# Kernel tuning notes

Measured on AMD Instinct MI355X. Metric: run time of the kernel, lower is better.

Reference implementation:

```python
import jax, jax.numpy as jnp
import numpy as np

B, S, D, H = 2, 2048, 1024, 16
DH = D // H  # 64


def setup_inputs() -> dict:
    key = jax.random.key(0)
    ks = jax.random.split(key, 9)
    def rn(k, shape, scale=1.0):
        return jax.random.normal(k, shape, dtype=jnp.float32) * scale
    w_scale = 1.0 / np.sqrt(D)
    return {
        "queries": rn(ks[0], (B, S, D)),
        "keys": rn(ks[1], (B, S, D)),
        "values": rn(ks[2], (B, S, D)),
        "Wq": rn(ks[3], (D, D), w_scale),
        "bq": rn(ks[4], (D,), w_scale),
        "Wk": rn(ks[5], (D, D), w_scale),
        "bk": rn(ks[6], (D,), w_scale),
        "Wv": rn(ks[7], (D, D), w_scale),
        "bv": rn(ks[8], (D,), w_scale),
    }


def _split_heads(x):
    # torch: cat(split(x, DH, dim=-1), dim=0) -> index (h*B + b); equivalent to
    # [B,S,H,DH] -> [H,B,S,DH]
    bsz, slen, _ = x.shape
    return x.reshape(bsz, slen, H, DH).transpose(2, 0, 1, 3)


def reference(queries, keys, values, Wq, bq, Wk, bk, Wv, bv):
    # Linear projections (W stored so that y = x @ W + b)
    Q = queries @ Wq + bq
    K = keys @ Wk + bk
    V = values @ Wv + bv

    Qh = _split_heads(Q)  # [H,B,S,DH]
    Kh = _split_heads(K)
    Vh = _split_heads(V)

    scale = 1.0 / jnp.sqrt(jnp.asarray(DH, dtype=Qh.dtype))
    scores = jnp.einsum("hbqd,hbkd->hbqk", Qh, Kh) * scale  # [H,B,S,S]
    attn = jax.nn.softmax(scores, axis=-1)  # dropout_rate=0 -> identity
    out = jnp.einsum("hbqk,hbkd->hbqd", attn, Vh)  # [H,B,S,DH]

    # torch: cat(split(out, B, dim=0), dim=2) -> [B,S,H*DH] with head h in slice h
    out = out.transpose(1, 2, 0, 3).reshape(queries.shape[0], queries.shape[1], D)
    return out + queries  # residual; NOTE: W_O is defined but unused in the original forward
```

## Files before the change

### kernel.cpp

```cpp
#include <hip/hip_runtime.h>
#include <hip/hip_bf16.h>
#include <math.h>

#define BB 2
#define SS 2048
#define DD 1024
#define HH 16
#define DHH 64
#define MM (BB * SS)

typedef float f32x4 __attribute__((ext_vector_type(4)));
typedef __bf16 bf16x8 __attribute__((ext_vector_type(8)));

#define N_QKV ((size_t)MM * DD)
#define N_W   ((size_t)DD * DD)

__device__ unsigned short g_X [3][N_QKV];
__device__ unsigned short g_Q [N_QKV];
__device__ unsigned short g_K [N_QKV];
__device__ unsigned short g_Vt[N_QKV];
__device__ unsigned short g_Wt[3][N_W];

__device__ __forceinline__ unsigned short f2bu(float f) {
    unsigned u = __float_as_uint(f);
    unsigned r = u + 0x7FFFu + ((u >> 16) & 1u);
    return (unsigned short)(r >> 16);
}

union FragU { uint4 u; bf16x8 v; unsigned short s[8]; };
static __device__ __forceinline__ bf16x8 ldfrag(const unsigned short* p) {
    FragU f; f.u = *(const uint4*)p; return f.v;
}

__global__ __launch_bounds__(256) void cvt3(
        const float* __restrict__ x0, const float* __restrict__ x1,
        const float* __restrict__ x2, unsigned short* __restrict__ X)
{
    const float* src = blockIdx.y == 0 ? x0 : (blockIdx.y == 1 ? x1 : x2);
    unsigned short* dst = X + (size_t)blockIdx.y * N_QKV;
    const size_t i = ((size_t)blockIdx.x * 256 + threadIdx.x) * 4;
    const float4 v = *(const float4*)(src + i);
    ushort4 s;
    s.x = f2bu(v.x); s.y = f2bu(v.y); s.z = f2bu(v.z); s.w = f2bu(v.w);
    *(ushort4*)(dst + i) = s;
}

__global__ __launch_bounds__(256) void transpose_w3(
        const float* __restrict__ W0, const float* __restrict__ W1,
        const float* __restrict__ W2, unsigned short* __restrict__ Wt3)
{
    const float* W = blockIdx.z == 0 ? W0 : (blockIdx.z == 1 ? W1 : W2);
    unsigned short* Wt = Wt3 + (size_t)blockIdx.z * N_W;
    __shared__ float Ts[64][65];
    const int t = threadIdx.x;
    const int k0 = blockIdx.y * 64, n0 = blockIdx.x * 64;
#pragma unroll
    for (int i = 0; i < 16; ++i) {
        const int f = t + 256 * i, r = f >> 6, c = f & 63;
        Ts[r][c] = W[(size_t)(k0 + r) * DD + n0 + c];
    }
    __syncthreads();
#pragma unroll
    for (int i = 0; i < 16; ++i) {
        const int f = t + 256 * i, r = f >> 6, c = f & 63;
        Wt[(size_t)(n0 + r) * DD + k0 + c] = f2bu(Ts[c][r]);
    }
}

__global__ __launch_bounds__(256) void proj3(
        const unsigned short* __restrict__ X, const unsigned short* __restrict__ Wt3,
        const float* __restrict__ bq, const float* __restrict__ bk,
        const float* __restrict__ bv,
        unsigned short* __restrict__ Qp, unsigned short* __restrict__ Kp,
        unsigned short* __restrict__ Vtp)
{
    const int z = blockIdx.z;
    const unsigned short* xb = X   + (size_t)z * N_QKV;
    const unsigned short* Wt = Wt3 + (size_t)z * N_W;
    const float* bias = z == 0 ? bq : (z == 1 ? bk : bv);
    const float scale = z == 0 ? 0.125f : 1.0f;

    __shared__ unsigned short As[128][72];
    __shared__ unsigned short Bs[128][72];
    const int t = threadIdx.x, lane = t & 63, w = t >> 6;
    const int q = lane >> 4, li = lane & 15;
    const int wm = (w >> 1) * 64, wn = (w & 1) * 64;
    const int m0 = blockIdx.y * 128, n0 = blockIdx.x * 128;
    const int rs = t >> 3, cs = (t & 7) * 8;

    f32x4 acc[4][4];
#pragma unroll
    for (int mt = 0; mt < 4; ++mt)
#pragma unroll
        for (int nt = 0; nt < 4; ++nt) acc[mt][nt] = (f32x4)0.f;

    uint4 pa0, pa1, pa2, pa3, pb0, pb1, pb2, pb3;
#define PROJ_LD(kk) \
    pa0 = *(const uint4*)(xb + (size_t)(m0 + rs      ) * DD + (kk) + cs); \
    pa1 = *(const uint4*)(xb + (size_t)(m0 + rs + 32 ) * DD + (kk) + cs); \
    pa2 = *(const uint4*)(xb + (size_t)(m0 + rs + 64 ) * DD + (kk) + cs); \
    pa3 = *(const uint4*)(xb + (size_t)(m0 + rs + 96 ) * DD + (kk) + cs); \
    pb0 = *(const uint4*)(Wt + (size_t)(n0 + rs      ) * DD + (kk) + cs); \
    pb1 = *(const uint4*)(Wt + (size_t)(n0 + rs + 32 ) * DD + (kk) + cs); \
    pb2 = *(const uint4*)(Wt + (size_t)(n0 + rs + 64 ) * DD + (kk) + cs); \
    pb3 = *(const uint4*)(Wt + (size_t)(n0 + rs + 96 ) * DD + (kk) + cs);

    PROJ_LD(0)

    for (int kk = 0; kk < DD; kk += 64) {
        *(uint4*)&As[rs     ][cs] = pa0;
        *(uint4*)&As[rs + 32][cs] = pa1;
        *(uint4*)&As[rs + 64][cs] = pa2;
        *(uint4*)&As[rs + 96][cs] = pa3;
        *(uint4*)&Bs[rs     ][cs] = pb0;
        *(uint4*)&Bs[rs + 32][cs] = pb1;
        *(uint4*)&Bs[rs + 64][cs] = pb2;
        *(uint4*)&Bs[rs + 96][cs] = pb3;
        __syncthreads();
        if (kk + 64 < DD) { PROJ_LD(kk + 64) }
#pragma unroll
        for (int ks = 0; ks < 64; ks += 32) {
            bf16x8 a[4], b[4];
#pragma unroll
            for (int mt = 0; mt < 4; ++mt) a[mt] = ldfrag(&As[wm + mt * 16 + li][ks + q * 8]);
#pragma unroll
            for (int nt = 0; nt < 4; ++nt) b[nt] = ldfrag(&Bs[wn + nt * 16 + li][ks + q * 8]);
#pragma unroll
            for (int mt = 0; mt < 4; ++mt)
#pragma unroll
                for (int nt = 0; nt < 4; ++nt)
                    acc[mt][nt] = __builtin_amdgcn_mfma_f32_16x16x32_bf16(
                        a[mt], b[nt], acc[mt][nt], 0, 0, 0);
        }
        __syncthreads();
    }
#undef PROJ_LD

    float bvv[4];
#pragma unroll
    for (int nt = 0; nt < 4; ++nt) bvv[nt] = bias[n0 + wn + nt * 16 + li];

    if (z < 2) {
        unsigned short* out = z == 0 ? Qp : Kp;
#pragma unroll
        for (int mt = 0; mt < 4; ++mt)
#pragma unroll
            for (int nt = 0; nt < 4; ++nt)
#pragma unroll
                for (int reg = 0; reg < 4; ++reg) {
                    const int m = m0 + wm + mt * 16 + q * 4 + reg;
                    out[(size_t)m * DD + n0 + wn + nt * 16 + li] =
                        f2bu((acc[mt][nt][reg] + bvv[nt]) * scale);
                }
    } else {
        const int b = m0 >> 11;
        const int h = (n0 + wn) >> 6;
#pragma unroll
        for (int mt = 0; mt < 4; ++mt)
#pragma unroll
            for (int nt = 0; nt < 4; ++nt) {
                const int s = (m0 & (SS - 1)) + wm + mt * 16 + q * 4;
                const int dh = nt * 16 + li;
                ushort4 sv;
                sv.x = f2bu(acc[mt][nt][0] + bvv[nt]);
                sv.y = f2bu(acc[mt][nt][1] + bvv[nt]);
                sv.z = f2bu(acc[mt][nt][2] + bvv[nt]);
                sv.w = f2bu(acc[mt][nt][3] + bvv[nt]);
                *(ushort4*)(Vtp + ((size_t)((b * HH + h) * DHH + dh)) * SS + s) = sv;
            }
    }
}

__global__ __launch_bounds__(256) void attn4(
        const unsigned short* __restrict__ Qg, const unsigned short* __restrict__ Kg,
        const unsigned short* __restrict__ Vtg,
        const float* __restrict__ queries, float* __restrict__ outp)
{
    __shared__ unsigned short QP [128][72];
    __shared__ unsigned short Ks [64][72];
    __shared__ unsigned short Vts[64][72];

    const int t = threadIdx.x, lane = t & 63, w = t >> 6;
    const int q = lane >> 4, li = lane & 15;
    const int qt = blockIdx.x, h = blockIdx.y, b = blockIdx.z;
    const int rs = t >> 3, cs = (t & 7) * 8;

    {
        const unsigned short* qsrc = Qg + (size_t)(b * SS + qt * 128) * DD + h * DHH + cs;
        *(uint4*)&QP[rs      ][cs] = *(const uint4*)(qsrc + (size_t)(rs      ) * DD);
        *(uint4*)&QP[rs + 32 ][cs] = *(const uint4*)(qsrc + (size_t)(rs + 32 ) * DD);
        *(uint4*)&QP[rs + 64 ][cs] = *(const uint4*)(qsrc + (size_t)(rs + 64 ) * DD);
        *(uint4*)&QP[rs + 96 ][cs] = *(const uint4*)(qsrc + (size_t)(rs + 96 ) * DD);
    }

    uint4 pk0, pk1, pv0, pv1;
#define ATTN_LD(s0) \
    pk0 = *(const uint4*)(Kg  + (size_t)(b * SS + (s0) + rs) * DD + h * DHH + cs); \
    pk1 = *(const uint4*)(Kg  + (size_t)(b * SS + (s0) + rs + 32) * DD + h * DHH + cs); \
    pv0 = *(const uint4*)(Vtg + ((size_t)((b * HH + h) * DHH + rs)) * SS + (s0) + cs); \
    pv1 = *(const uint4*)(Vtg + ((size_t)((b * HH + h) * DHH + rs + 32)) * SS + (s0) + cs);

    ATTN_LD(0)
    *(uint4*)&Ks [rs     ][cs] = pk0;
    *(uint4*)&Ks [rs + 32][cs] = pk1;
    *(uint4*)&Vts[rs     ][cs] = pv0;
    *(uint4*)&Vts[rs + 32][cs] = pv1;
    __syncthreads();

    bf16x8 qa[2][2];
#pragma unroll
    for (int mt = 0; mt < 2; ++mt)
#pragma unroll
        for (int ki = 0; ki < 2; ++ki)
            qa[mt][ki] = ldfrag(&QP[w * 32 + mt * 16 + li][ki * 32 + q * 8]);

    FragU ones;
#pragma unroll
    for (int j = 0; j < 8; ++j) ones.s[j] = 0x3F80;

    f32x4 o[2][4], lacc[2];
#pragma unroll
    for (int mt = 0; mt < 2; ++mt) {
        lacc[mt] = (f32x4)0.f;
#pragma unroll
        for (int nt = 0; nt < 4; ++nt) o[mt][nt] = (f32x4)0.f;
    }

    for (int kt = 0; kt < SS / 64; ++kt) {
        if (kt + 1 < SS / 64) { ATTN_LD((kt + 1) * 64) }

        f32x4 sc[2][4];
#pragma unroll
        for (int mt = 0; mt < 2; ++mt)
#pragma unroll
            for (int nt = 0; nt < 4; ++nt) sc[mt][nt] = (f32x4)0.f;
#pragma unroll
        for (int ki = 0; ki < 2; ++ki) {
            bf16x8 bb[4];
#pragma unroll
            for (int nt = 0; nt < 4; ++nt)
                bb[nt] = ldfrag(&Ks[nt * 16 + li][ki * 32 + q * 8]);
#pragma unroll
            for (int mt = 0; mt < 2; ++mt)
#pragma unroll
                for (int nt = 0; nt < 4; ++nt)
                    sc[mt][nt] = __builtin_amdgcn_mfma_f32_16x16x32_bf16(
                        qa[mt][ki], bb[nt], sc[mt][nt], 0, 0, 0);
        }

#pragma unroll
        for (int mt = 0; mt < 2; ++mt)
#pragma unroll
            for (int nt = 0; nt < 4; ++nt)
#pragma unroll
                for (int reg = 0; reg < 4; ++reg)
                    QP[w * 32 + mt * 16 + q * 4 + reg][nt * 16 + li] =
                        f2bu(__expf(sc[mt][nt][reg]));

#pragma unroll
        for (int ki = 0; ki < 2; ++ki) {
            bf16x8 vb[4];
#pragma unroll
            for (int nt = 0; nt < 4; ++nt)
                vb[nt] = ldfrag(&Vts[nt * 16 + li][ki * 32 + q * 8]);
#pragma unroll
            for (int mt = 0; mt < 2; ++mt) {
                const bf16x8 Pa = ldfrag(&QP[w * 32 + mt * 16 + li][ki * 32 + q * 8]);
#pragma unroll
                for (int nt = 0; nt < 4; ++nt)
                    o[mt][nt] = __builtin_amdgcn_mfma_f32_16x16x32_bf16(
                        Pa, vb[nt], o[mt][nt], 0, 0, 0);
                lacc[mt] = __builtin_amdgcn_mfma_f32_16x16x32_bf16(
                    Pa, ones.v, lacc[mt], 0, 0, 0);
            }
        }
        __syncthreads();
        if (kt + 1 < SS / 64) {
            *(uint4*)&Ks [rs     ][cs] = pk0;
            *(uint4*)&Ks [rs + 32][cs] = pk1;
            *(uint4*)&Vts[rs     ][cs] = pv0;
            *(uint4*)&Vts[rs + 32][cs] = pv1;
        }
        __syncthreads();
    }
#undef ATTN_LD

#pragma unroll
    for (int mt = 0; mt < 2; ++mt) {
        float inv[4];
#pragma unroll
        for (int reg = 0; reg < 4; ++reg) inv[reg] = 1.f / lacc[mt][reg];
#pragma unroll
        for (int nt = 0; nt < 4; ++nt)
#pragma unroll
            for (int reg = 0; reg < 4; ++reg) {
                const size_t g = (size_t)(b * SS + qt * 128 + w * 32 + mt * 16 + q * 4 + reg) * DD
                               + h * DHH + nt * 16 + li;
                outp[g] = o[mt][nt][reg] * inv[reg] + queries[g];
            }
    }
}

extern "C" void kernel_launch(void* const* d_in, const int* in_sizes, int n_in,
                              void* d_out, int out_size, void* d_ws, size_t ws_size,
                              hipStream_t stream) {
    const float* queries = (const float*)d_in[0];
    const float* keys    = (const float*)d_in[1];
    const float* values  = (const float*)d_in[2];
    const float* Wq      = (const float*)d_in[3];
    const float* bq      = (const float*)d_in[4];
    const float* Wk      = (const float*)d_in[5];
    const float* bk      = (const float*)d_in[6];
    const float* Wv      = (const float*)d_in[7];
    const float* bv      = (const float*)d_in[8];
    float* outp = (float*)d_out;

    const size_t need = (6 * N_QKV + 3 * N_W) * sizeof(unsigned short);
    unsigned short *Xp, *Qp, *Kp, *Vtp, *Wtp;
    if (ws_size >= need) {
        Xp  = (unsigned short*)d_ws;
        Qp  = Xp + 3 * N_QKV;
        Kp  = Qp + N_QKV;
        Vtp = Kp + N_QKV;
        Wtp = Vtp + N_QKV;
    } else {
        hipGetSymbolAddress((void**)&Xp,  HIP_SYMBOL(g_X));
        hipGetSymbolAddress((void**)&Qp,  HIP_SYMBOL(g_Q));
        hipGetSymbolAddress((void**)&Kp,  HIP_SYMBOL(g_K));
        hipGetSymbolAddress((void**)&Vtp, HIP_SYMBOL(g_Vt));
        hipGetSymbolAddress((void**)&Wtp, HIP_SYMBOL(g_Wt));
    }

    const dim3 bp(256);
    cvt3<<<dim3(MM * DD / 1024, 3), bp, 0, stream>>>(queries, keys, values, Xp);
    transpose_w3<<<dim3(16, 16, 3), bp, 0, stream>>>(Wq, Wk, Wv, Wtp);
    proj3<<<dim3(8, 32, 3), bp, 0, stream>>>(Xp, Wtp, bq, bk, bv, Qp, Kp, Vtp);
    attn4<<<dim3(SS / 128, HH, BB), bp, 0, stream>>>(Qp, Kp, Vtp, queries, outp);
}
```

Measured before the change: 211.0 us.

## Rewrite attention with 32x32 MFMA, register-resident P, swizzled double-buffered K/V

The attention kernel is rebuilt around 32x32x16 bf16 MFMAs. S^T is computed so the probabilities stay in registers and are exchanged across half-waves with shuffles instead of a round-trip through shared memory. K/V tiles are double-buffered in XOR-swizzled LDS, which removes one barrier per iteration. The Q scale folds in log2(e) so exp2f can be used, and row sums are accumulated in scalar registers rather than with a ones-MFMA. These changes aim to cut LDS traffic, barriers and wasted MFMA work, at the cost of more complex lane mapping. Like the previous code, there is still no max subtraction, so overflow safety depends on the score range.

```diff
diff --git a/kernel.cpp b/kernel.cpp
--- a/kernel.cpp
+++ b/kernel.cpp
@@ -10,6 +10,7 @@
 #define MM (BB * SS)
 
 typedef float f32x4 __attribute__((ext_vector_type(4)));
+typedef float f32x16 __attribute__((ext_vector_type(16)));
 typedef __bf16 bf16x8 __attribute__((ext_vector_type(8)));
 
 #define N_QKV ((size_t)MM * DD)
@@ -30,6 +31,12 @@
 union FragU { uint4 u; bf16x8 v; unsigned short s[8]; };
 static __device__ __forceinline__ bf16x8 ldfrag(const unsigned short* p) {
     FragU f; f.u = *(const uint4*)p; return f.v;
+}
+
+static __device__ __forceinline__ unsigned pkbf(float a, float b) {
+    union { __bf16 h[2]; unsigned u; } w;
+    w.h[0] = (__bf16)a; w.h[1] = (__bf16)b;
+    return w.u;
 }
 
 __global__ __launch_bounds__(256) void cvt3(
@@ -78,7 +85,7 @@
     const unsigned short* xb = X   + (size_t)z * N_QKV;
     const unsigned short* Wt = Wt3 + (size_t)z * N_W;
     const float* bias = z == 0 ? bq : (z == 1 ? bk : bv);
-    const float scale = z == 0 ? 0.125f : 1.0f;
+    const float scale = z == 0 ? 0.18033688011112042f : 1.0f;
 
     __shared__ unsigned short As[128][72];
     __shared__ unsigned short Bs[128][72];
@@ -171,133 +178,122 @@
     }
 }
 
-__global__ __launch_bounds__(256) void attn4(
+__global__ __launch_bounds__(256) void attn5(
         const unsigned short* __restrict__ Qg, const unsigned short* __restrict__ Kg,
         const unsigned short* __restrict__ Vtg,
         const float* __restrict__ queries, float* __restrict__ outp)
 {
-    __shared__ unsigned short QP [128][72];
-    __shared__ unsigned short Ks [64][72];
-    __shared__ unsigned short Vts[64][72];
+    __shared__ unsigned short Kb[2][64][64];
+    __shared__ unsigned short Vb[2][64][64];
+    __shared__ float invL[4][32];
 
     const int t = threadIdx.x, lane = t & 63, w = t >> 6;
-    const int q = lane >> 4, li = lane & 15;
+    const int col = lane & 31;
+    const int hi  = lane >> 5;
     const int qt = blockIdx.x, h = blockIdx.y, b = blockIdx.z;
-    const int rs = t >> 3, cs = (t & 7) * 8;
-
+
+    const int sr = t >> 3;
+    const int sc = t & 7;
+
+    const unsigned short* Kbase = Kg  + (size_t)(b * SS) * DD + h * DHH;
+    const unsigned short* Vbase = Vtg + ((size_t)((b * HH + h) * DHH)) * SS;
+
+    bf16x8 qa[4];
     {
-        const unsigned short* qsrc = Qg + (size_t)(b * SS + qt * 128) * DD + h * DHH + cs;
-        *(uint4*)&QP[rs      ][cs] = *(const uint4*)(qsrc + (size_t)(rs      ) * DD);
-        *(uint4*)&QP[rs + 32 ][cs] = *(const uint4*)(qsrc + (size_t)(rs + 32 ) * DD);
-        *(uint4*)&QP[rs + 64 ][cs] = *(const uint4*)(qsrc + (size_t)(rs + 64 ) * DD);
-        *(uint4*)&QP[rs + 96 ][cs] = *(const uint4*)(qsrc + (size_t)(rs + 96 ) * DD);
-    }
-
-    uint4 pk0, pk1, pv0, pv1;
-#define ATTN_LD(s0) \
-    pk0 = *(const uint4*)(Kg  + (size_t)(b * SS + (s0) + rs) * DD + h * DHH + cs); \
-    pk1 = *(const uint4*)(Kg  + (size_t)(b * SS + (s0) + rs + 32) * DD + h * DHH + cs); \
-    pv0 = *(const uint4*)(Vtg + ((size_t)((b * HH + h) * DHH + rs)) * SS + (s0) + cs); \
-    pv1 = *(const uint4*)(Vtg + ((size_t)((b * HH + h) * DHH + rs + 32)) * SS + (s0) + cs);
-
-    ATTN_LD(0)
-    *(uint4*)&Ks [rs     ][cs] = pk0;
-    *(uint4*)&Ks [rs + 32][cs] = pk1;
-    *(uint4*)&Vts[rs     ][cs] = pv0;
-    *(uint4*)&Vts[rs + 32][cs] = pv1;
+        const unsigned short* qp =
+            Qg + (size_t)(b * SS + qt * 128 + w * 32 + col) * DD + h * DHH + hi * 8;
+#pragma unroll
+        for (int i = 0; i < 4; ++i) qa[i] = ldfrag(qp + i * 16);
+    }
+
+    f32x16 o0 = (f32x16)0.f, o1 = (f32x16)0.f;
+    float lsum = 0.f;
+
+    uint4 k0, k1, v0, v1;
+#define LD_TILE(s0) \
+    k0 = *(const uint4*)(Kbase + (size_t)((s0) + sr     ) * DD + sc * 8); \
+    k1 = *(const uint4*)(Kbase + (size_t)((s0) + sr + 32) * DD + sc * 8); \
+    v0 = *(const uint4*)(Vbase + (size_t)(sr     ) * SS + (s0) + sc * 8); \
+    v1 = *(const uint4*)(Vbase + (size_t)(sr + 32) * SS + (s0) + sc * 8);
+
+#define ST_TILE(buf) \
+    *(uint4*)&Kb[buf][sr     ][(sc ^ (sr & 7)) * 8] = k0; \
+    *(uint4*)&Kb[buf][sr + 32][(sc ^ (sr & 7)) * 8] = k1; \
+    *(uint4*)&Vb[buf][sr     ][(sc ^ (sr & 7)) * 8] = v0; \
+    *(uint4*)&Vb[buf][sr + 32][(sc ^ (sr & 7)) * 8] = v1;
+
+    LD_TILE(0)
+    ST_TILE(0)
     __syncthreads();
 
-    bf16x8 qa[2][2];
-#pragma unroll
-    for (int mt = 0; mt < 2; ++mt)
-#pragma unroll
-        for (int ki = 0; ki < 2; ++ki)
-            qa[mt][ki] = ldfrag(&QP[w * 32 + mt * 16 + li][ki * 32 + q * 8]);
-
-    FragU ones;
-#pragma unroll
-    for (int j = 0; j < 8; ++j) ones.s[j] = 0x3F80;
-
-    f32x4 o[2][4], lacc[2];
-#pragma unroll
-    for (int mt = 0; mt < 2; ++mt) {
-        lacc[mt] = (f32x4)0.f;
-#pragma unroll
-        for (int nt = 0; nt < 4; ++nt) o[mt][nt] = (f32x4)0.f;
-    }
-
-    for (int kt = 0; kt < SS / 64; ++kt) {
-        if (kt + 1 < SS / 64) { ATTN_LD((kt + 1) * 64) }
-
-        f32x4 sc[2][4];
-#pragma unroll
-        for (int mt = 0; mt < 2; ++mt)
-#pragma unroll
-            for (int nt = 0; nt < 4; ++nt) sc[mt][nt] = (f32x4)0.f;
-#pragma unroll
-        for (int ki = 0; ki < 2; ++ki) {
-            bf16x8 bb[4];
-#pragma unroll
-            for (int nt = 0; nt < 4; ++nt)
-                bb[nt] = ldfrag(&Ks[nt * 16 + li][ki * 32 + q * 8]);
-#pragma unroll
-            for (int mt = 0; mt < 2; ++mt)
-#pragma unroll
-                for (int nt = 0; nt < 4; ++nt)
-                    sc[mt][nt] = __builtin_amdgcn_mfma_f32_16x16x32_bf16(
-                        qa[mt][ki], bb[nt], sc[mt][nt], 0, 0, 0);
-        }
-
-#pragma unroll
-        for (int mt = 0; mt < 2; ++mt)
-#pragma unroll
-            for (int nt = 0; nt < 4; ++nt)
-#pragma unroll
-                for (int reg = 0; reg < 4; ++reg)
-                    QP[w * 32 + mt * 16 + q * 4 + reg][nt * 16 + li] =
-                        f2bu(__expf(sc[mt][nt][reg]));
-
-#pragma unroll
-        for (int ki = 0; ki < 2; ++ki) {
-            bf16x8 vb[4];
-#pragma unroll
-            for (int nt = 0; nt < 4; ++nt)
-                vb[nt] = ldfrag(&Vts[nt * 16 + li][ki * 32 + q * 8]);
-#pragma unroll
-            for (int mt = 0; mt < 2; ++mt) {
-                const bf16x8 Pa = ldfrag(&QP[w * 32 + mt * 16 + li][ki * 32 + q * 8]);
-#pragma unroll
-                for (int nt = 0; nt < 4; ++nt)
-                    o[mt][nt] = __builtin_amdgcn_mfma_f32_16x16x32_bf16(
-                        Pa, vb[nt], o[mt][nt], 0, 0, 0);
-                lacc[mt] = __builtin_amdgcn_mfma_f32_16x16x32_bf16(
-                    Pa, ones.v, lacc[mt], 0, 0, 0);
+    const int NT = SS / 64;
+    for (int kt = 0; kt < NT; ++kt) {
+        const int cur = kt & 1;
+        if (kt + 1 < NT) { LD_TILE((kt + 1) * 64) }
+
+#pragma unroll
+        for (int ksub = 0; ksub < 2; ++ksub) {
+            f32x16 st = (f32x16)0.f;
+            const int krow = ksub * 32 + col;
+#pragma unroll
+            for (int i = 0; i < 4; ++i) {
+                bf16x8 ka = ldfrag(&Kb[cur][krow][((i * 2 + hi) ^ (krow & 7)) * 8]);
+                st = __builtin_amdgcn_mfma_f32_32x32x16_bf16(ka, qa[i], st, 0, 0, 0);
+            }
+
+            float pe[16];
+#pragma unroll
+            for (int r = 0; r < 16; ++r) { pe[r] = exp2f(st[r]); lsum += pe[r]; }
+
+            unsigned wl[2][2], wh[2][2];
+#pragma unroll
+            for (int s = 0; s < 2; ++s) {
+                wl[s][0] = pkbf(pe[8 * s + 0], pe[8 * s + 1]);
+                wl[s][1] = pkbf(pe[8 * s + 2], pe[8 * s + 3]);
+                wh[s][0] = pkbf(pe[8 * s + 4], pe[8 * s + 5]);
+                wh[s][1] = pkbf(pe[8 * s + 6], pe[8 * s + 7]);
+            }
+
+            if (ksub == 0 && kt + 1 < NT) { ST_TILE(cur ^ 1) }
+
+#pragma unroll
+            for (int s = 0; s < 2; ++s) {
+                const unsigned self0 = hi ? wh[s][0] : wl[s][0];
+                const unsigned self1 = hi ? wh[s][1] : wl[s][1];
+                const unsigned send0 = hi ? wl[s][0] : wh[s][0];
+                const unsigned send1 = hi ? wl[s][1] : wh[s][1];
+                const unsigned r0 = (unsigned)__shfl_xor((int)send0, 32);
+                const unsigned r1 = (unsigned)__shfl_xor((int)send1, 32);
+                FragU pf;
+                pf.u.x = hi ? r0 : self0;
+                pf.u.y = hi ? r1 : self1;
+                pf.u.z = hi ? self0 : r0;
+                pf.u.w = hi ? self1 : r1;
+
+                const int vslot = ksub * 4 + s * 2 + hi;
+                bf16x8 vb0 = ldfrag(&Vb[cur][col     ][(vslot ^ (col & 7)) * 8]);
+                bf16x8 vb1 = ldfrag(&Vb[cur][col + 32][(vslot ^ (col & 7)) * 8]);
+                o0 = __builtin_amdgcn_mfma_f32_32x32x16_bf16(pf.v, vb0, o0, 0, 0, 0);
+                o1 = __builtin_amdgcn_mfma_f32_32x32x16_bf16(pf.v, vb1, o1, 0, 0, 0);
             }
         }
         __syncthreads();
-        if (kt + 1 < SS / 64) {
-            *(uint4*)&Ks [rs     ][cs] = pk0;
-            *(uint4*)&Ks [rs + 32][cs] = pk1;
-            *(uint4*)&Vts[rs     ][cs] = pv0;
-            *(uint4*)&Vts[rs + 32][cs] = pv1;
-        }
-        __syncthreads();
-    }
-#undef ATTN_LD
-
-#pragma unroll
-    for (int mt = 0; mt < 2; ++mt) {
-        float inv[4];
-#pragma unroll
-        for (int reg = 0; reg < 4; ++reg) inv[reg] = 1.f / lacc[mt][reg];
-#pragma unroll
-        for (int nt = 0; nt < 4; ++nt)
-#pragma unroll
-            for (int reg = 0; reg < 4; ++reg) {
-                const size_t g = (size_t)(b * SS + qt * 128 + w * 32 + mt * 16 + q * 4 + reg) * DD
-                               + h * DHH + nt * 16 + li;
-                outp[g] = o[mt][nt][reg] * inv[reg] + queries[g];
-            }
+    }
+#undef LD_TILE
+#undef ST_TILE
+
+    const float lt = lsum + __shfl_xor(lsum, 32);
+    if (lane < 32) invL[w][lane] = 1.f / lt;
+    __syncthreads();
+
+    const size_t gbase = (size_t)(b * SS + qt * 128 + w * 32) * DD + h * DHH + col;
+#pragma unroll
+    for (int reg = 0; reg < 16; ++reg) {
+        const int rl = (reg & 3) + 8 * (reg >> 2) + 4 * hi;
+        const float inv = invL[w][rl];
+        const size_t g = gbase + (size_t)rl * DD;
+        outp[g]      = o0[reg] * inv + queries[g];
+        outp[g + 32] = o1[reg] * inv + queries[g + 32];
     }
 }
 
@@ -335,5 +331,5 @@
     cvt3<<<dim3(MM * DD / 1024, 3), bp, 0, stream>>>(queries, keys, values, Xp);
     transpose_w3<<<dim3(16, 16, 3), bp, 0, stream>>>(Wq, Wk, Wv, Wtp);
     proj3<<<dim3(8, 32, 3), bp, 0, stream>>>(Xp, Wtp, bq, bk, bv, Qp, Kp, Vtp);
-    attn4<<<dim3(SS / 128, HH, BB), bp, 0, stream>>>(Qp, Kp, Vtp, queries, outp);
-}
+    attn5<<<dim3(SS / 128, HH, BB), bp, 0, stream>>>(Qp, Kp, Vtp, queries, outp);
+}
```

After: 220.6 us. 1.05x slower.
